# Kernel tuning notes

Measured on AMD Instinct MI355X. Metric: run time of the kernel, lower is better.

The kernel has to match this reference:

```python
import jax, jax.numpy as jnp
import numpy as np

T_MAX = 16           # max target instance label (labels 1..T_MAX, 0 = background)
CCL_ITERS = 128      # fixed label-propagation iterations for connected components
S1 = 0.7310585786300049    # sigmoid(1.0)
SP0 = 0.6931471805599453   # softplus(0.0) = log 2
SP1 = 1.3132616875182228   # softplus(1.0)


def bce_dice(logits, target):
    # BCEDiceLoss: BCE-with-logits (mean) + soft dice on sigmoid probs
    p = jax.nn.sigmoid(logits)
    bce = jnp.mean(jax.nn.softplus(logits) - logits * target)
    inter = jnp.sum(p * target)
    dice = 1.0 - (2.0 * inter + 1.0) / (jnp.sum(p) + jnp.sum(target) + 1.0)
    return bce + dice


def connected_components(mask):
    # 4-connected components via iterative max-label propagation.
    # mask: [B,H,W] bool. Returns int32 label map; component id = max flat index in component + 1.
    B, H, W = mask.shape
    init = jnp.where(mask, jnp.arange(1, B * H * W + 1, dtype=jnp.int32).reshape(B, H, W), 0)

    def step(lab, _):
        up = jnp.pad(lab, ((0, 0), (1, 0), (0, 0)))[:, :H, :]
        dn = jnp.pad(lab, ((0, 0), (0, 1), (0, 0)))[:, 1:, :]
        lf = jnp.pad(lab, ((0, 0), (0, 0), (1, 0)))[:, :, :W]
        rt = jnp.pad(lab, ((0, 0), (0, 0), (0, 1)))[:, :, 1:]
        nb = jnp.maximum(jnp.maximum(up, dn), jnp.maximum(lf, rt))
        return jnp.where(mask, jnp.maximum(lab, nb), 0), None

    lab, _ = jax.lax.scan(step, init, None, length=CCL_ITERS)
    return lab


def _forward(pred_out, target_mask):
    B, C, H, W = pred_out.shape
    N = B * H * W
    Nf = jnp.float32(N)

    pm = jnp.argmax(pred_out, axis=1)          # [B,H,W] in {0,1} since C=2
    fg = pm > 0                                 # predicted foreground

    # base loss on channel-1 logits masked to predicted foreground vs binarized target
    res = bce_dice(pred_out[:, 1:2] * fg[:, None].astype(pred_out.dtype),
                   (target_mask > 0).astype(jnp.float32))

    # relabel predicted foreground into connected components (global unique ids)
    lab = connected_components(fg)              # [B,H,W]
    comp = jnp.where(fg, lab - 1, 0).reshape(-1)          # component root id in [0,N)
    tgt = target_mask[:, 0].reshape(-1).astype(jnp.int32)  # target label 0..T_MAX
    w = fg.reshape(-1).astype(jnp.float32)

    # confusion counts: inter[p, t] = |{pixels: pred comp p AND target label t}|
    inter = jax.ops.segment_sum(w, comp * (T_MAX + 1) + tgt,
                                num_segments=N * (T_MAX + 1)).reshape(N, T_MAX + 1)
    cnt_p = inter.sum(axis=1)                                       # [N] pred comp sizes
    cnt_t = jax.ops.segment_sum(jnp.ones((N,), jnp.float32), tgt,
                                num_segments=T_MAX + 1)             # [T+1] target sizes

    def pair_losses(inter_t, ct):
        # BCEDice between binary comp mask (as logits in {0,1}) and binary target mask,
        # expressed in closed form from the confusion counts.
        bce = (Nf * SP0 + cnt_p * (SP1 - SP0) - inter_t) / Nf
        sum_pt = 0.5 * ct + (S1 - 0.5) * inter_t
        sum_p = 0.5 * Nf + (S1 - 0.5) * cnt_p
        dice = 1.0 - (2.0 * sum_pt + 1.0) / (sum_p + ct + 1.0)
        return bce + dice

    def step(carry, t):
        used, acc, matched, un_tgt = carry
        ct = cnt_t[t]
        present = ct > 0
        avail = (cnt_p > 0) & (~used)
        any_avail = jnp.any(avail)
        losses = jnp.where(avail, pair_losses(inter[:, t], ct), jnp.inf)
        idx = jnp.argmin(losses)
        do = present & any_avail
        acc = acc + jnp.where(do, losses[idx], 0.0)
        used = used.at[idx].set(used[idx] | do)
        matched = matched + do.astype(jnp.float32)
        un_tgt = un_tgt + (present & (~any_avail)).astype(jnp.float32)
        return (used, acc, matched, un_tgt), None

    carry0 = (jnp.zeros((N,), bool), res, jnp.float32(0.0), jnp.float32(0.0))
    (used, acc, matched, un_tgt), _ = jax.lax.scan(step, carry0, jnp.arange(1, T_MAX + 1))

    n_pred = jnp.sum((cnt_p > 0).astype(jnp.float32))   # total pred components
    return acc + (n_pred - matched) + un_tgt            # penalties for unmatched comps/targets


def setup_inputs() -> dict:
    key = jax.random.key(0)
    k1, k2 = jax.random.split(key)
    pred_out = jax.random.normal(k1, (4, 2, 512, 512), dtype=jnp.float32)
    target_mask = jax.random.randint(k2, (4, 1, 512, 512), 0, 17, dtype=jnp.int32)
    return {"pred_out": pred_out, "target_mask": target_mask}


def reference(pred_out, target_mask):
    return _forward(pred_out, target_mask)
```

## Files before the change

### kernel.cpp

```cpp
#include <hip/hip_runtime.h>
#include <math.h>

#define HH 512
#define WW 512
#define HWSZ (HH * WW)
#define NB 4
#define NPIX (NB * HWSZ)
#define TMAX 16

#define CAP 131072
#define NPART 24
#define NBLK 1024
#define SBLK 512

#define TS 32
#define SEAMS 15
#define EDGES_PER_DIR (NB * SEAMS * HH)
#define NEDGES (2 * EDGES_PER_DIR)
#define BORDER_BLOCKS 64

struct Scalars {
  double sums[4];
  int cnt_t[TMAX + 1];
  int n_comp;
};

__device__ __forceinline__ float pair_loss(float cp, float it, float ctf) {
  const float Nf = (float)NPIX;
  float bce = (Nf * 0.69314718f + cp * 0.62011451f - it) / Nf;
  float sum_pt = 0.5f * ctf + 0.23105858f * it;
  float sum_p = 0.5f * Nf + 0.23105858f * cp;
  float dice = 1.0f - (2.0f * sum_pt + 1.0f) / (sum_p + ctf + 1.0f);
  return bce + dice;
}

__device__ __forceinline__ int chaseRO(const int* __restrict__ P, int x) {
  int p = P[x];
  while (p != x) { x = p; p = P[x]; }
  return x;
}
__device__ __forceinline__ int findRootH(int* P, int x) {
  int p = P[x];
  while (p != x) {
    int gp = P[p];
    if (gp == p) return p;
    P[x] = gp;
    x = gp; p = P[x];
  }
  return x;
}
__device__ void unite(int* P, int a, int b) {
  a = findRootH(P, a);
  b = findRootH(P, b);
  for (;;) {
    if (a == b) return;
    if (a > b) { int t = a; a = b; b = t; }
    int old = atomicMax(&P[a], b);
    if (old == a) return;
    a = findRootH(P, old);
    b = findRootH(P, b);
  }
}
__device__ __forceinline__ int findL(const int* lp, int x) {
  int p = lp[x];
  while (p != x) { x = p; p = lp[x]; }
  return x;
}
__device__ void uniteL(int* lp, int a, int b) {
  a = findL(lp, a);
  b = findL(lp, b);
  for (;;) {
    if (a == b) return;
    if (a > b) { int t = a; a = b; b = t; }
    int old = atomicMax(&lp[a], b);
    if (old == a) return;
    a = findL(lp, old);
    b = findL(lp, b);
  }
}

__global__ __launch_bounds__(256) void k_init(const float* __restrict__ pred,
                                              const int* __restrict__ tgt,
                                              int* __restrict__ P,
                                              int* __restrict__ cnt,
                                              double* __restrict__ part) {
  __shared__ int hist[TMAX + 1];
  __shared__ double red[4][4];
  int tid = threadIdx.x;
  if (tid <= TMAX) hist[tid] = 0;
  __syncthreads();
  int g = blockIdx.x * 256 + tid;
  int i = g << 2;
  int b = i >> 18;
  int hw = i & (HWSZ - 1);
  const float* pb = pred + ((size_t)(b << 1)) * HWSZ;
  float4 p0 = *(const float4*)(pb + hw);
  float4 p1 = *(const float4*)(pb + HWSZ + hw);
  int4 tv = *(const int4*)(tgt + i);
  int4 lv;
  float s0 = 0.f, s1 = 0.f, s2 = 0.f, s3 = 0.f;
#define ELEM(P0, P1, TV, IDX, LOUT)                              \
  {                                                              \
    bool fg = (P1) > (P0);                                       \
    float logit = fg ? (P1) : 0.0f;                              \
    float tb = ((TV) > 0) ? 1.0f : 0.0f;                         \
    float sp = fmaxf(logit, 0.0f) + log1pf(expf(-fabsf(logit))); \
    s0 += sp - logit * tb;                                       \
    float pr = 1.0f / (1.0f + expf(-logit));                     \
    s1 += pr; s2 += pr * tb; s3 += tb;                           \
    atomicAdd(&hist[TV], 1);                                     \
    LOUT = fg ? (IDX) : -1;                                      \
  }
  ELEM(p0.x, p1.x, tv.x, i + 0, lv.x)
  ELEM(p0.y, p1.y, tv.y, i + 1, lv.y)
  ELEM(p0.z, p1.z, tv.z, i + 2, lv.z)
  ELEM(p0.w, p1.w, tv.w, i + 3, lv.w)
#undef ELEM
  *(int4*)(P + i) = lv;
  *(int4*)(cnt + i) = make_int4(0, 0, 0, 0);
  for (int o = 32; o > 0; o >>= 1) {
    s0 += __shfl_down(s0, o);
    s1 += __shfl_down(s1, o);
    s2 += __shfl_down(s2, o);
    s3 += __shfl_down(s3, o);
  }
  int lane = tid & 63, wid = tid >> 6;
  if (!lane) { red[wid][0] = s0; red[wid][1] = s1; red[wid][2] = s2; red[wid][3] = s3; }
  __syncthreads();
  double* row = part + (size_t)blockIdx.x * NPART;
  if (tid <= TMAX) row[4 + tid] = (double)hist[tid];
  if (!tid) {
    row[0] = red[0][0] + red[1][0] + red[2][0] + red[3][0];
    row[1] = red[0][1] + red[1][1] + red[2][1] + red[3][1];
    row[2] = red[0][2] + red[1][2] + red[2][2] + red[3][2];
    row[3] = red[0][3] + red[1][3] + red[2][3] + red[3][3];
  }
}

__global__ __launch_bounds__(256) void k_local(int* __restrict__ P,
                                               int* __restrict__ cnt) {
  __shared__ int lp[TS * TS];
  __shared__ int sz[TS * TS];
  int tid = threadIdx.x;
  int bid = blockIdx.x;
  int b = bid >> 8;
  int ty = (bid >> 4) & 15, tx = bid & 15;
  int gbase = b * HWSZ + ((ty << 5) << 9) + (tx << 5);

#pragma unroll
  for (int k = 0; k < 4; ++k) {
    int c = (k << 8) + tid;
    int r = c >> 5, q = c & 31;
    int gi = gbase + (r << 9) + q;
    lp[c] = (P[gi] >= 0) ? c : -1;
    sz[c] = 0;
  }
  __syncthreads();
#pragma unroll
  for (int k = 0; k < 4; ++k) {
    int c = (k << 8) + tid;
    if (lp[c] >= 0) {
      int r = c >> 5, q = c & 31;
      if (q < TS - 1 && lp[c + 1] >= 0)  uniteL(lp, c, c + 1);
      if (r < TS - 1 && lp[c + TS] >= 0) uniteL(lp, c, c + TS);
    }
  }
  __syncthreads();
  int rootc[4];
#pragma unroll
  for (int k = 0; k < 4; ++k) {
    int c = (k << 8) + tid;
    if (lp[c] >= 0) {
      int rr = findL(lp, c);
      rootc[k] = rr;
      atomicAdd(&sz[rr], 1);
    } else rootc[k] = -1;
  }
  __syncthreads();
#pragma unroll
  for (int k = 0; k < 4; ++k) {
    int c = (k << 8) + tid;
    int rr = rootc[k];
    if (rr >= 0) {
      int r = c >> 5, q = c & 31;
      int gi = gbase + (r << 9) + q;
      int groot = gbase + ((rr >> 5) << 9) + (rr & 31);
      P[gi] = groot;
      if (c == rr) cnt[gi] = sz[c];
    }
  }
}

__global__ __launch_bounds__(256) void k_border(int* __restrict__ P,
                                                const double* __restrict__ part,
                                                Scalars* __restrict__ sc) {
  int tid = threadIdx.x;
  int bid = blockIdx.x;
  if (bid == 0) {
    int lane = tid & 63, wv = tid >> 6;
    double v[21];
#pragma unroll
    for (int j = 0; j < 21; ++j) v[j] = 0.0;
    for (int r = tid; r < NBLK; r += 256) {
      const double* row = part + (size_t)r * NPART;
#pragma unroll
      for (int j = 0; j < 21; ++j) v[j] += row[j];
    }
#pragma unroll
    for (int o = 32; o > 0; o >>= 1) {
#pragma unroll
      for (int j = 0; j < 21; ++j) v[j] += __shfl_down(v[j], o);
    }
    __shared__ double redr[4][21];
    if (!lane) {
#pragma unroll
      for (int j = 0; j < 21; ++j) redr[wv][j] = v[j];
    }
    __syncthreads();
    if (!tid) {
#pragma unroll
      for (int j = 0; j < 21; ++j) v[j] = redr[0][j] + redr[1][j] + redr[2][j] + redr[3][j];
      sc->sums[0] = v[0]; sc->sums[1] = v[1]; sc->sums[2] = v[2]; sc->sums[3] = v[3];
      for (int j = 0; j <= TMAX; ++j) sc->cnt_t[j] = (int)(v[4 + j] + 0.5);
    }
  }
  for (int e = bid * 256 + tid; e < NEDGES; e += BORDER_BLOCKS * 256) {
    int dir = e >= EDGES_PER_DIR;
    int e2 = dir ? e - EDGES_PER_DIR : e;
    int b = e2 / (SEAMS * HH);
    int r2 = e2 - b * (SEAMS * HH);
    int seam = r2 >> 9;
    int pos = r2 & 511;
    int i, j;
    if (!dir) {
      int w = (TS - 1) + (seam << 5);
      i = b * HWSZ + (pos << 9) + w;
      j = i + 1;
    } else {
      int h = (TS - 1) + (seam << 5);
      i = b * HWSZ + (h << 9) + pos;
      j = i + WW;
    }
    if (P[i] >= 0 && P[j] >= 0) unite(P, i, j);
  }
}

__global__ __launch_bounds__(256) void k_flat(int* __restrict__ P,
                                              int* __restrict__ cnt,
                                              int* __restrict__ interD) {
  int g = blockIdx.x * 256 + threadIdx.x;
  *(int4*)(interD + ((size_t)g << 3)) = make_int4(0, 0, 0, 0);
  *(int4*)(interD + ((size_t)g << 3) + 4) = make_int4(0, 0, 0, 0);
  int i0 = g << 2;
  int4 pv = *(const int4*)(P + i0);
  int4 cv = *(const int4*)(cnt + i0);
  int4 rv;
  rv.x = (pv.x < 0) ? -1 : chaseRO(P, pv.x);
  rv.y = (pv.y < 0) ? -1 : chaseRO(P, pv.y);
  rv.z = (pv.z < 0) ? -1 : chaseRO(P, pv.z);
  rv.w = (pv.w < 0) ? -1 : chaseRO(P, pv.w);
  *(int4*)(P + i0) = rv;
  if (cv.x > 0 && rv.x != i0 + 0) { atomicAdd(&cnt[rv.x], cv.x); cnt[i0 + 0] = 0; }
  if (cv.y > 0 && rv.y != i0 + 1) { atomicAdd(&cnt[rv.y], cv.y); cnt[i0 + 1] = 0; }
  if (cv.z > 0 && rv.z != i0 + 2) { atomicAdd(&cnt[rv.z], cv.z); cnt[i0 + 2] = 0; }
  if (cv.w > 0 && rv.w != i0 + 3) { atomicAdd(&cnt[rv.w], cv.w); cnt[i0 + 3] = 0; }
}

__global__ __launch_bounds__(256) void k_bcnt(const int* __restrict__ cnt,
                                              int* __restrict__ bcnt) {
  __shared__ int redi[4];
  int tid = threadIdx.x;
  int base = blockIdx.x << 10;
  int4 cv = *(const int4*)(cnt + base + (tid << 2));
  int c = (cv.x > 0) + (cv.y > 0) + (cv.z > 0) + (cv.w > 0);
  for (int o = 32; o > 0; o >>= 1) c += __shfl_down(c, o);
  int lane = tid & 63, wv = tid >> 6;
  if (!lane) redi[wv] = c;
  __syncthreads();
  if (!tid) bcnt[blockIdx.x] = redi[0] + redi[1] + redi[2] + redi[3];
}

__global__ __launch_bounds__(256) void k_scatter(int* __restrict__ cnt,
                                                 const int* __restrict__ bcnt,
                                                 int* __restrict__ cntD,
                                                 Scalars* __restrict__ sc) {
  __shared__ int redi[4];
  __shared__ int redp4[4];
  __shared__ int wtot[4];
  int tid = threadIdx.x;
  int bid = blockIdx.x;
  int lane = tid & 63, wv = tid >> 6;
  int base = bid << 10;
  int4 cv = *(const int4*)(cnt + base + (tid << 2));
  int val[4] = { cv.x, cv.y, cv.z, cv.w };
  int cme = (cv.x > 0) + (cv.y > 0) + (cv.z > 0) + (cv.w > 0);
  int4 bv = *(const int4*)(bcnt + (tid << 2));
  int j0 = tid << 2;
  int tot = bv.x + bv.y + bv.z + bv.w;
  int pre = ((j0 + 0 < bid) ? bv.x : 0) + ((j0 + 1 < bid) ? bv.y : 0)
          + ((j0 + 2 < bid) ? bv.z : 0) + ((j0 + 3 < bid) ? bv.w : 0);
  for (int o = 32; o > 0; o >>= 1) {
    tot += __shfl_down(tot, o);
    pre += __shfl_down(pre, o);
  }
  if (!lane) { redi[wv] = tot; redp4[wv] = pre; }
  __syncthreads();
  tot = redi[0] + redi[1] + redi[2] + redi[3];
  pre = redp4[0] + redp4[1] + redp4[2] + redp4[3];
  if (bid == 0 && tid == 0) sc->n_comp = tot;
  int v = cme;
  for (int o = 1; o < 64; o <<= 1) {
    int u = __shfl_up(v, o);
    if (lane >= o) v += u;
  }
  if (lane == 63) wtot[wv] = v;
  __syncthreads();
  int add = 0;
  for (int w = 0; w < wv; ++w) add += wtot[w];
  int d = pre + v + add - cme;
#pragma unroll
  for (int k = 0; k < 4; ++k) {
    int c = val[k];
    if (c > 0) {
      if (d < CAP) cntD[d] = c;
      cnt[base + (tid << 2) + k] = d;
      ++d;
    }
  }
}

__global__ __launch_bounds__(256) void k_interall(const int* __restrict__ P,
                                                  const int* __restrict__ tgt,
                                                  const int* __restrict__ dense_of,
                                                  int* __restrict__ interD) {
  int g = blockIdx.x * 256 + threadIdx.x;
  int i0 = g << 2;
  int4 rv = *(const int4*)(P + i0);
  int4 tv = *(const int4*)(tgt + i0);
#define DO(R, T)                                                     \
  if ((R) >= 0 && (T)) {                                             \
    int dd = dense_of[R];                                            \
    if ((unsigned)dd < CAP) atomicAdd(&interD[((size_t)dd << 4) + (T) - 1], 1); \
  }
  DO(rv.x, tv.x) DO(rv.y, tv.y) DO(rv.z, tv.z) DO(rv.w, tv.w)
#undef DO
}

__global__ __launch_bounds__(256) void k_scanmins(const Scalars* __restrict__ sc,
                                                  const int* __restrict__ cntD,
                                                  const int* __restrict__ interD,
                                                  unsigned long long* __restrict__ bm) {
  int tid = threadIdx.x;
  int d = blockIdx.x * 256 + tid;
  int n_comp = sc->n_comp;
  int c = (d < n_comp) ? cntD[d] : 0;
  int itv[16];
  if (c > 0) {
#pragma unroll
    for (int k = 0; k < 4; ++k) {
      int4 r = *(const int4*)(interD + ((size_t)d << 4) + (k << 2));
      itv[(k << 2) + 0] = r.x; itv[(k << 2) + 1] = r.y;
      itv[(k << 2) + 2] = r.z; itv[(k << 2) + 3] = r.w;
    }
  }
  __shared__ unsigned long long wmin[4][16];
  float cp = (float)c;
  int lane = tid & 63, wv = tid >> 6;
#pragma unroll
  for (int t = 0; t < 16; ++t) {
    unsigned long long key = ~0ULL;
    if (c > 0) {
      float loss = pair_loss(cp, (float)itv[t], (float)sc->cnt_t[t + 1]);
      key = ((unsigned long long)__float_as_uint(loss) << 32) | (unsigned)d;
    }
    for (int o = 32; o > 0; o >>= 1) {
      unsigned long long kk = __shfl_down(key, o);
      if (kk < key) key = kk;
    }
    if (!lane) wmin[wv][t] = key;
  }
  __syncthreads();
  if (tid < 16) {
    unsigned long long m = wmin[0][tid];
    if (wmin[1][tid] < m) m = wmin[1][tid];
    if (wmin[2][tid] < m) m = wmin[2][tid];
    if (wmin[3][tid] < m) m = wmin[3][tid];
    bm[(size_t)tid * SBLK + blockIdx.x] = m;
  }
}

__global__ __launch_bounds__(1024) void k_greedy(const Scalars* __restrict__ sc,
                                                 const int* __restrict__ cntD,
                                                 const int* __restrict__ interD,
                                                 const unsigned long long* __restrict__ bm,
                                                 float* __restrict__ out) {
  __shared__ unsigned long long lbm[16 * SBLK];
  int tid = threadIdx.x;
  int lane = tid & 63;
#pragma unroll
  for (int k = 0; k < 8; ++k) lbm[tid + (k << 10)] = bm[tid + (k << 10)];
  __syncthreads();

  int n_comp = sc->n_comp;
  if (n_comp > CAP) n_comp = CAP;
  double acc = 0.0;
  int matched = 0, un = 0, nused = 0;
  int used_reg = -1;

  for (int t = 1; t <= TMAX; ++t) {
    int ct = sc->cnt_t[t];
    if (ct == 0) continue;
    const int rowoff = (t - 1) * SBLK;
    for (int iter = 0; iter < 40; ++iter) {
      unsigned long long key = lbm[rowoff + lane];
#pragma unroll
      for (int k = 1; k < 8; ++k) {
        unsigned long long kk = lbm[rowoff + lane + (k << 6)];
        if (kk < key) key = kk;
      }
      for (int o = 32; o > 0; o >>= 1) {
        unsigned long long kk = __shfl_xor(key, o);
        if (kk < key) key = kk;
      }
      if (key == ~0ULL) { un += 1; break; }
      int dd = (int)(key & 0xFFFFFFFFu);
      bool ex = false;
      for (int u = 0; u < nused; ++u) {
        int uid = __shfl(used_reg, u);
        if (uid == dd) { ex = true; break; }
      }
      if (!ex) {
        acc += (double)__uint_as_float((unsigned)(key >> 32));
        matched += 1;
        if (lane == nused) used_reg = dd;
        nused += 1;
        break;
      }
      int b = dd >> 8;
      unsigned long long nk = ~0ULL;
#pragma unroll
      for (int k = 0; k < 4; ++k) {
        int d2 = (b << 8) + lane + (k << 6);
        int c = (d2 < n_comp) ? cntD[d2] : 0;
        if (c > 0) {
          bool ex2 = false;
          for (int u = 0; u < nused; ++u) {
            int uid = __shfl(used_reg, u);
            if (uid == d2) { ex2 = true; break; }
          }
          if (!ex2) {
            float loss = pair_loss((float)c, (float)interD[((size_t)d2 << 4) + (t - 1)], (float)ct);
            unsigned long long cand = ((unsigned long long)__float_as_uint(loss) << 32) | (unsigned)d2;
            if (cand < nk) nk = cand;
          }
        }
      }
      for (int o = 32; o > 0; o >>= 1) {
        unsigned long long kk = __shfl_xor(nk, o);
        if (kk < nk) nk = kk;
      }
      __syncthreads();
      if (!tid) lbm[rowoff + b] = nk;
      __syncthreads();
    }
  }

  if (!tid) {
    double Nd = (double)NPIX;
    double res = sc->sums[0] / Nd
               + 1.0 - (2.0 * sc->sums[2] + 1.0) / (sc->sums[1] + sc->sums[3] + 1.0);
    out[0] = (float)(res + acc + (double)(n_comp - matched) + (double)un);
  }
}

extern "C" void kernel_launch(void* const* d_in, const int* in_sizes, int n_in,
                              void* d_out, int out_size, void* d_ws, size_t ws_size,
                              hipStream_t stream) {
  (void)in_sizes; (void)n_in; (void)out_size; (void)ws_size;
  const float* pred = (const float*)d_in[0];
  const int* tgt = (const int*)d_in[1];
  float* out = (float*)d_out;

  char* w = (char*)d_ws;
  int* P     = (int*)w;            w += (size_t)NPIX * 4;
  int* cnt   = (int*)w;            w += (size_t)NPIX * 4;
  double* part = (double*)w;       w += (size_t)NBLK * NPART * 8;
  Scalars* sc = (Scalars*)w;       w += 256;
  int* bcnt  = (int*)w;            w += 4096;
  int* cntD  = (int*)w;            w += (size_t)CAP * 4;
  unsigned long long* bm = (unsigned long long*)w; w += (size_t)16 * SBLK * 8;
  int* interD = (int*)w;

  k_init<<<NBLK, 256, 0, stream>>>(pred, tgt, P, cnt, part);
  k_local<<<NBLK, 256, 0, stream>>>(P, cnt);
  k_border<<<BORDER_BLOCKS, 256, 0, stream>>>(P, part, sc);
  k_flat<<<NBLK, 256, 0, stream>>>(P, cnt, interD);
  k_bcnt<<<NBLK, 256, 0, stream>>>(cnt, bcnt);
  k_scatter<<<NBLK, 256, 0, stream>>>(cnt, bcnt, cntD, sc);
  k_interall<<<NBLK, 256, 0, stream>>>(P, tgt, cnt, interD);
  k_scanmins<<<SBLK, 256, 0, stream>>>(sc, cntD, interD, bm);
  k_greedy<<<1, 1024, 0, stream>>>(sc, cntD, interD, bm, out);
}
```

Measured before the change: 130.5 us.

## Fuse init with tile-local CCL and derive component sizes from intersection rows

```diff
diff --git a/kernel.cpp b/kernel.cpp
--- a/kernel.cpp
+++ b/kernel.cpp
@@ -12,6 +12,7 @@
 #define NPART 24
 #define NBLK 1024
 #define SBLK 512
+#define RSTRIDE 20
 
 #define TS 32
 #define SEAMS 15
@@ -79,27 +80,29 @@
   }
 }
 
-__global__ __launch_bounds__(256) void k_init(const float* __restrict__ pred,
+__global__ __launch_bounds__(256) void k_tile(const float* __restrict__ pred,
                                               const int* __restrict__ tgt,
                                               int* __restrict__ P,
-                                              int* __restrict__ cnt,
                                               double* __restrict__ part) {
+  __shared__ int lp[TS * TS];
   __shared__ int hist[TMAX + 1];
   __shared__ double red[4][4];
-  int tid = threadIdx.x;
+  int tid = threadIdx.x, bid = blockIdx.x;
   if (tid <= TMAX) hist[tid] = 0;
-  __syncthreads();
-  int g = blockIdx.x * 256 + tid;
-  int i = g << 2;
-  int b = i >> 18;
-  int hw = i & (HWSZ - 1);
+  int b = bid >> 8;
+  int ty = (bid >> 4) & 15, tx = bid & 15;
+  int gbase = b * HWSZ + ((ty << 5) << 9) + (tx << 5);
+  int c0 = tid << 2;
+  int hw0 = (gbase - b * HWSZ) + ((c0 >> 5) << 9) + (c0 & 31);
+  int gi0 = b * HWSZ + hw0;
   const float* pb = pred + ((size_t)(b << 1)) * HWSZ;
-  float4 p0 = *(const float4*)(pb + hw);
-  float4 p1 = *(const float4*)(pb + HWSZ + hw);
-  int4 tv = *(const int4*)(tgt + i);
-  int4 lv;
+  float4 p0 = *(const float4*)(pb + hw0);
+  float4 p1 = *(const float4*)(pb + HWSZ + hw0);
+  int4 tv = *(const int4*)(tgt + gi0);
+  __syncthreads();
+
   float s0 = 0.f, s1 = 0.f, s2 = 0.f, s3 = 0.f;
-#define ELEM(P0, P1, TV, IDX, LOUT)                              \
+#define ELEM(P0, P1, TV, K)                                      \
   {                                                              \
     bool fg = (P1) > (P0);                                       \
     float logit = fg ? (P1) : 0.0f;                              \
@@ -109,15 +112,37 @@
     float pr = 1.0f / (1.0f + expf(-logit));                     \
     s1 += pr; s2 += pr * tb; s3 += tb;                           \
     atomicAdd(&hist[TV], 1);                                     \
-    LOUT = fg ? (IDX) : -1;                                      \
-  }
-  ELEM(p0.x, p1.x, tv.x, i + 0, lv.x)
-  ELEM(p0.y, p1.y, tv.y, i + 1, lv.y)
-  ELEM(p0.z, p1.z, tv.z, i + 2, lv.z)
-  ELEM(p0.w, p1.w, tv.w, i + 3, lv.w)
+    lp[c0 + (K)] = fg ? (c0 + (K)) : -1;                         \
+  }
+  ELEM(p0.x, p1.x, tv.x, 0)
+  ELEM(p0.y, p1.y, tv.y, 1)
+  ELEM(p0.z, p1.z, tv.z, 2)
+  ELEM(p0.w, p1.w, tv.w, 3)
 #undef ELEM
-  *(int4*)(P + i) = lv;
-  *(int4*)(cnt + i) = make_int4(0, 0, 0, 0);
+  __syncthreads();
+
+#pragma unroll
+  for (int k = 0; k < 4; ++k) {
+    int c = (k << 8) + tid;
+    if (lp[c] >= 0) {
+      int r = c >> 5, q = c & 31;
+      if (q < TS - 1 && lp[c + 1] >= 0)  uniteL(lp, c, c + 1);
+      if (r < TS - 1 && lp[c + TS] >= 0) uniteL(lp, c, c + TS);
+    }
+  }
+  __syncthreads();
+#pragma unroll
+  for (int k = 0; k < 4; ++k) {
+    int c = (k << 8) + tid;
+    int gi = gbase + ((c >> 5) << 9) + (c & 31);
+    if (lp[c] >= 0) {
+      int rr = findL(lp, c);
+      P[gi] = gbase + ((rr >> 5) << 9) + (rr & 31);
+    } else {
+      P[gi] = -1;
+    }
+  }
+
   for (int o = 32; o > 0; o >>= 1) {
     s0 += __shfl_down(s0, o);
     s1 += __shfl_down(s1, o);
@@ -127,67 +152,13 @@
   int lane = tid & 63, wid = tid >> 6;
   if (!lane) { red[wid][0] = s0; red[wid][1] = s1; red[wid][2] = s2; red[wid][3] = s3; }
   __syncthreads();
-  double* row = part + (size_t)blockIdx.x * NPART;
+  double* row = part + (size_t)bid * NPART;
   if (tid <= TMAX) row[4 + tid] = (double)hist[tid];
   if (!tid) {
     row[0] = red[0][0] + red[1][0] + red[2][0] + red[3][0];
     row[1] = red[0][1] + red[1][1] + red[2][1] + red[3][1];
     row[2] = red[0][2] + red[1][2] + red[2][2] + red[3][2];
     row[3] = red[0][3] + red[1][3] + red[2][3] + red[3][3];
-  }
-}
-
-__global__ __launch_bounds__(256) void k_local(int* __restrict__ P,
-                                               int* __restrict__ cnt) {
-  __shared__ int lp[TS * TS];
-  __shared__ int sz[TS * TS];
-  int tid = threadIdx.x;
-  int bid = blockIdx.x;
-  int b = bid >> 8;
-  int ty = (bid >> 4) & 15, tx = bid & 15;
-  int gbase = b * HWSZ + ((ty << 5) << 9) + (tx << 5);
-
-#pragma unroll
-  for (int k = 0; k < 4; ++k) {
-    int c = (k << 8) + tid;
-    int r = c >> 5, q = c & 31;
-    int gi = gbase + (r << 9) + q;
-    lp[c] = (P[gi] >= 0) ? c : -1;
-    sz[c] = 0;
-  }
-  __syncthreads();
-#pragma unroll
-  for (int k = 0; k < 4; ++k) {
-    int c = (k << 8) + tid;
-    if (lp[c] >= 0) {
-      int r = c >> 5, q = c & 31;
-      if (q < TS - 1 && lp[c + 1] >= 0)  uniteL(lp, c, c + 1);
-      if (r < TS - 1 && lp[c + TS] >= 0) uniteL(lp, c, c + TS);
-    }
-  }
-  __syncthreads();
-  int rootc[4];
-#pragma unroll
-  for (int k = 0; k < 4; ++k) {
-    int c = (k << 8) + tid;
-    if (lp[c] >= 0) {
-      int rr = findL(lp, c);
-      rootc[k] = rr;
-      atomicAdd(&sz[rr], 1);
-    } else rootc[k] = -1;
-  }
-  __syncthreads();
-#pragma unroll
-  for (int k = 0; k < 4; ++k) {
-    int c = (k << 8) + tid;
-    int rr = rootc[k];
-    if (rr >= 0) {
-      int r = c >> 5, q = c & 31;
-      int gi = gbase + (r << 9) + q;
-      int groot = gbase + ((rr >> 5) << 9) + (rr & 31);
-      P[gi] = groot;
-      if (c == rr) cnt[gi] = sz[c];
-    }
   }
 }
 
@@ -245,34 +216,20 @@
   }
 }
 
-__global__ __launch_bounds__(256) void k_flat(int* __restrict__ P,
-                                              int* __restrict__ cnt,
-                                              int* __restrict__ interD) {
-  int g = blockIdx.x * 256 + threadIdx.x;
-  *(int4*)(interD + ((size_t)g << 3)) = make_int4(0, 0, 0, 0);
-  *(int4*)(interD + ((size_t)g << 3) + 4) = make_int4(0, 0, 0, 0);
+__global__ __launch_bounds__(256) void k_flatb(int* __restrict__ P,
+                                               int* __restrict__ bcnt) {
+  __shared__ int redi[4];
+  int tid = threadIdx.x;
+  int g = blockIdx.x * 256 + tid;
   int i0 = g << 2;
   int4 pv = *(const int4*)(P + i0);
-  int4 cv = *(const int4*)(cnt + i0);
   int4 rv;
   rv.x = (pv.x < 0) ? -1 : chaseRO(P, pv.x);
   rv.y = (pv.y < 0) ? -1 : chaseRO(P, pv.y);
   rv.z = (pv.z < 0) ? -1 : chaseRO(P, pv.z);
   rv.w = (pv.w < 0) ? -1 : chaseRO(P, pv.w);
   *(int4*)(P + i0) = rv;
-  if (cv.x > 0 && rv.x != i0 + 0) { atomicAdd(&cnt[rv.x], cv.x); cnt[i0 + 0] = 0; }
-  if (cv.y > 0 && rv.y != i0 + 1) { atomicAdd(&cnt[rv.y], cv.y); cnt[i0 + 1] = 0; }
-  if (cv.z > 0 && rv.z != i0 + 2) { atomicAdd(&cnt[rv.z], cv.z); cnt[i0 + 2] = 0; }
-  if (cv.w > 0 && rv.w != i0 + 3) { atomicAdd(&cnt[rv.w], cv.w); cnt[i0 + 3] = 0; }
-}
-
-__global__ __launch_bounds__(256) void k_bcnt(const int* __restrict__ cnt,
-                                              int* __restrict__ bcnt) {
-  __shared__ int redi[4];
-  int tid = threadIdx.x;
-  int base = blockIdx.x << 10;
-  int4 cv = *(const int4*)(cnt + base + (tid << 2));
-  int c = (cv.x > 0) + (cv.y > 0) + (cv.z > 0) + (cv.w > 0);
+  int c = (rv.x == i0 + 0) + (rv.y == i0 + 1) + (rv.z == i0 + 2) + (rv.w == i0 + 3);
   for (int o = 32; o > 0; o >>= 1) c += __shfl_down(c, o);
   int lane = tid & 63, wv = tid >> 6;
   if (!lane) redi[wv] = c;
@@ -280,9 +237,10 @@
   if (!tid) bcnt[blockIdx.x] = redi[0] + redi[1] + redi[2] + redi[3];
 }
 
-__global__ __launch_bounds__(256) void k_scatter(int* __restrict__ cnt,
+__global__ __launch_bounds__(256) void k_scatter(const int* __restrict__ P,
                                                  const int* __restrict__ bcnt,
-                                                 int* __restrict__ cntD,
+                                                 int* __restrict__ dof,
+                                                 int* __restrict__ interD,
                                                  Scalars* __restrict__ sc) {
   __shared__ int redi[4];
   __shared__ int redp4[4];
@@ -290,10 +248,10 @@
   int tid = threadIdx.x;
   int bid = blockIdx.x;
   int lane = tid & 63, wv = tid >> 6;
-  int base = bid << 10;
-  int4 cv = *(const int4*)(cnt + base + (tid << 2));
-  int val[4] = { cv.x, cv.y, cv.z, cv.w };
-  int cme = (cv.x > 0) + (cv.y > 0) + (cv.z > 0) + (cv.w > 0);
+  int i0 = (bid << 10) + (tid << 2);
+  int4 rv = *(const int4*)(P + i0);
+  int isr[4] = { rv.x == i0 + 0, rv.y == i0 + 1, rv.z == i0 + 2, rv.w == i0 + 3 };
+  int cme = isr[0] + isr[1] + isr[2] + isr[3];
   int4 bv = *(const int4*)(bcnt + (tid << 2));
   int j0 = tid << 2;
   int tot = bv.x + bv.y + bv.z + bv.w;
@@ -320,64 +278,67 @@
   int d = pre + v + add - cme;
 #pragma unroll
   for (int k = 0; k < 4; ++k) {
-    int c = val[k];
-    if (c > 0) {
-      if (d < CAP) cntD[d] = c;
-      cnt[base + (tid << 2) + k] = d;
-      ++d;
-    }
-  }
+    if (isr[k]) { dof[i0 + k] = d; ++d; }
+  }
+  int btot = wtot[0] + wtot[1] + wtot[2] + wtot[3];
+  size_t zs = (size_t)pre * RSTRIDE;
+  size_t ze = (size_t)(pre + btot) * RSTRIDE;
+  size_t zcap = (size_t)CAP * RSTRIDE;
+  if (ze > zcap) ze = zcap;
+  for (size_t j = zs + tid; j < ze; j += 256) interD[j] = 0;
 }
 
 __global__ __launch_bounds__(256) void k_interall(const int* __restrict__ P,
                                                   const int* __restrict__ tgt,
-                                                  const int* __restrict__ dense_of,
+                                                  const int* __restrict__ dof,
                                                   int* __restrict__ interD) {
   int g = blockIdx.x * 256 + threadIdx.x;
   int i0 = g << 2;
   int4 rv = *(const int4*)(P + i0);
   int4 tv = *(const int4*)(tgt + i0);
 #define DO(R, T)                                                     \
-  if ((R) >= 0 && (T)) {                                             \
-    int dd = dense_of[R];                                            \
-    if ((unsigned)dd < CAP) atomicAdd(&interD[((size_t)dd << 4) + (T) - 1], 1); \
+  if ((R) >= 0) {                                                    \
+    int dd = dof[R];                                                 \
+    if ((unsigned)dd < CAP) atomicAdd(&interD[(size_t)dd * RSTRIDE + (T)], 1); \
   }
   DO(rv.x, tv.x) DO(rv.y, tv.y) DO(rv.z, tv.z) DO(rv.w, tv.w)
 #undef DO
 }
 
 __global__ __launch_bounds__(256) void k_scanmins(const Scalars* __restrict__ sc,
-                                                  const int* __restrict__ cntD,
                                                   const int* __restrict__ interD,
                                                   unsigned long long* __restrict__ bm) {
   int tid = threadIdx.x;
   int d = blockIdx.x * 256 + tid;
   int n_comp = sc->n_comp;
-  int c = (d < n_comp) ? cntD[d] : 0;
-  int itv[16];
-  if (c > 0) {
-#pragma unroll
-    for (int k = 0; k < 4; ++k) {
-      int4 r = *(const int4*)(interD + ((size_t)d << 4) + (k << 2));
-      itv[(k << 2) + 0] = r.x; itv[(k << 2) + 1] = r.y;
-      itv[(k << 2) + 2] = r.z; itv[(k << 2) + 3] = r.w;
+  if (n_comp > CAP) n_comp = CAP;
+  int row[RSTRIDE];
+  int cp = 0;
+  if (d < n_comp) {
+    const int4* rp = (const int4*)(interD + (size_t)d * RSTRIDE);
+#pragma unroll
+    for (int k = 0; k < 5; ++k) {
+      int4 r4 = rp[k];
+      row[(k << 2) + 0] = r4.x; row[(k << 2) + 1] = r4.y;
+      row[(k << 2) + 2] = r4.z; row[(k << 2) + 3] = r4.w;
+      cp += r4.x + r4.y + r4.z + r4.w;
     }
   }
   __shared__ unsigned long long wmin[4][16];
-  float cp = (float)c;
+  float cpf = (float)cp;
   int lane = tid & 63, wv = tid >> 6;
 #pragma unroll
-  for (int t = 0; t < 16; ++t) {
+  for (int t = 1; t <= TMAX; ++t) {
     unsigned long long key = ~0ULL;
-    if (c > 0) {
-      float loss = pair_loss(cp, (float)itv[t], (float)sc->cnt_t[t + 1]);
+    if (d < n_comp) {
+      float loss = pair_loss(cpf, (float)row[t], (float)sc->cnt_t[t]);
       key = ((unsigned long long)__float_as_uint(loss) << 32) | (unsigned)d;
     }
     for (int o = 32; o > 0; o >>= 1) {
       unsigned long long kk = __shfl_down(key, o);
       if (kk < key) key = kk;
     }
-    if (!lane) wmin[wv][t] = key;
+    if (!lane) wmin[wv][t - 1] = key;
   }
   __syncthreads();
   if (tid < 16) {
@@ -390,7 +351,6 @@
 }
 
 __global__ __launch_bounds__(1024) void k_greedy(const Scalars* __restrict__ sc,
-                                                 const int* __restrict__ cntD,
                                                  const int* __restrict__ interD,
                                                  const unsigned long long* __restrict__ bm,
                                                  float* __restrict__ out) {
@@ -441,15 +401,18 @@
 #pragma unroll
       for (int k = 0; k < 4; ++k) {
         int d2 = (b << 8) + lane + (k << 6);
-        int c = (d2 < n_comp) ? cntD[d2] : 0;
-        if (c > 0) {
+        if (d2 < n_comp) {
           bool ex2 = false;
           for (int u = 0; u < nused; ++u) {
             int uid = __shfl(used_reg, u);
             if (uid == d2) { ex2 = true; break; }
           }
           if (!ex2) {
-            float loss = pair_loss((float)c, (float)interD[((size_t)d2 << 4) + (t - 1)], (float)ct);
+            const int* rrow = interD + (size_t)d2 * RSTRIDE;
+            int c = 0;
+#pragma unroll
+            for (int j = 0; j < RSTRIDE; ++j) c += rrow[j];
+            float loss = pair_loss((float)c, (float)rrow[t], (float)ct);
             unsigned long long cand = ((unsigned long long)__float_as_uint(loss) << 32) | (unsigned)d2;
             if (cand < nk) nk = cand;
           }
@@ -483,21 +446,18 @@
 
   char* w = (char*)d_ws;
   int* P     = (int*)w;            w += (size_t)NPIX * 4;
-  int* cnt   = (int*)w;            w += (size_t)NPIX * 4;
+  int* dof   = (int*)w;            w += (size_t)NPIX * 4;
   double* part = (double*)w;       w += (size_t)NBLK * NPART * 8;
   Scalars* sc = (Scalars*)w;       w += 256;
   int* bcnt  = (int*)w;            w += 4096;
-  int* cntD  = (int*)w;            w += (size_t)CAP * 4;
   unsigned long long* bm = (unsigned long long*)w; w += (size_t)16 * SBLK * 8;
   int* interD = (int*)w;
 
-  k_init<<<NBLK, 256, 0, stream>>>(pred, tgt, P, cnt, part);
-  k_local<<<NBLK, 256, 0, stream>>>(P, cnt);
+  k_tile<<<NBLK, 256, 0, stream>>>(pred, tgt, P, part);
   k_border<<<BORDER_BLOCKS, 256, 0, stream>>>(P, part, sc);
-  k_flat<<<NBLK, 256, 0, stream>>>(P, cnt, interD);
-  k_bcnt<<<NBLK, 256, 0, stream>>>(cnt, bcnt);
-  k_scatter<<<NBLK, 256, 0, stream>>>(cnt, bcnt, cntD, sc);
-  k_interall<<<NBLK, 256, 0, stream>>>(P, tgt, cnt, interD);
-  k_scanmins<<<SBLK, 256, 0, stream>>>(sc, cntD, interD, bm);
-  k_greedy<<<1, 1024, 0, stream>>>(sc, cntD, interD, bm, out);
-}
+  k_flatb<<<NBLK, 256, 0, stream>>>(P, bcnt);
+  k_scatter<<<NBLK, 256, 0, stream>>>(P, bcnt, dof, interD, sc);
+  k_interall<<<NBLK, 256, 0, stream>>>(P, tgt, dof, interD);
+  k_scanmins<<<SBLK, 256, 0, stream>>>(sc, interD, bm);
+  k_greedy<<<1, 1024, 0, stream>>>(sc, interD, bm, out);
+}
```

New measurement: 124.6 us. -4.5%, faster.
